# Optimization experiments

Hardware: AMD Instinct MI355X
Metric: run time of the kernel (lower is better)

The kernel has to match this reference:

```python
import jax, jax.numpy as jnp
import numpy as np

NPERSEG = 128  # filter_size


def setup_inputs() -> dict:
    key = jax.random.key(0)
    x = jax.random.normal(key, (32, 64, 16384), dtype=jnp.float32)
    return {"x": x}


def _welch_psd(x):
    # window=None -> rectangular, scaling = sum(ones^2) = NPERSEG, fs = 1.0
    step = NPERSEG // 2          # noverlap = nperseg // 2
    T = x.shape[-1]
    num_segments = (T - step) // step
    # frame the signal: [B, C, S, NPERSEG]
    idx = jnp.arange(num_segments)[:, None] * step + jnp.arange(NPERSEG)
    segs = x[..., idx]
    segs = segs - jnp.mean(segs, axis=-1, keepdims=True)
    seg_fft = jnp.fft.rfft(segs, axis=-1)
    psd = (jnp.abs(seg_fft) ** 2) / NPERSEG
    # nperseg even -> double all bins except DC and Nyquist
    factor = jnp.ones((psd.shape[-1],), dtype=psd.dtype).at[1:-1].set(2.0)
    psd = psd * factor
    return jnp.mean(psd, axis=-2)  # average over segments -> [B, C, F]


def reference(x):
    psd = _welch_psd(x)                       # [B, C, F], F = 65
    F_bins = psd.shape[-1]
    sqrt_psd = jnp.sqrt(psd)
    # weights = 1 / F (faithful to original: divides by psd.shape[-1])
    barycenter = jnp.sum(sqrt_psd / F_bins, axis=0) ** 2   # [C, F] (first_iter)
    D = jnp.sqrt(barycenter)[None] / sqrt_psd              # [B, C, F]
    H = jnp.fft.irfft(D, axis=-1)                          # [B, C, 2*(F-1)=128]
    H = jnp.fft.fftshift(H, axes=-1)
    H = jnp.flip(H, axis=-1)
    B, C, T = x.shape
    K = H.shape[-1]
    # per-sample depthwise conv1d, padding='same' (torch even-kernel: left=(K-1)//2, right=K-1-left)
    left = (K - 1) // 2
    out = jax.lax.conv_general_dilated(
        x.reshape(1, B * C, T),
        H.reshape(B * C, 1, K),
        window_strides=(1,),
        padding=[(left, K - 1 - left)],
        feature_group_count=B * C,
    )
    return out.reshape(B, C, T)
```

## Files before the change

kernel.cpp:

```cpp
#include <hip/hip_runtime.h>
#include <math.h>

#define NCH   2048
#define TLEN  16384
#define NSEG  255
#define NF    65

__device__ __forceinline__ int swzA(int i) {
    return (i & ~63) | ((i & 63) ^ ((i >> 6) & 31));
}
__host__ __device__ constexpr int br6(int i) {
    return ((i & 1) << 5) | ((i & 2) << 3) | ((i & 4) << 1) |
           ((i & 8) >> 1) | ((i & 16) >> 3) | ((i & 32) >> 5);
}

__attribute__((amdgpu_flat_work_group_size(256, 256), amdgpu_waves_per_eu(2, 2)))
__global__ void psd_kernel(const float* __restrict__ x, float* __restrict__ psd_g) {
    __shared__ float xl[TLEN];
    const int ch  = blockIdx.x;
    const int tid = threadIdx.x;
    const float4* __restrict__ x4 = reinterpret_cast<const float4*>(x) + (size_t)ch * (TLEN / 4);
#pragma unroll
    for (int it = 0; it < 16; ++it) {
        int i4 = it * 256 + tid;
        float4 v = x4[i4];
        int i = i4 << 2;
        xl[swzA(i + 0)] = v.x;
        xl[swzA(i + 1)] = v.y;
        xl[swzA(i + 2)] = v.z;
        xl[swzA(i + 3)] = v.w;
    }
    __syncthreads();

    const int   seg   = (tid < NSEG) ? tid : (NSEG - 1);
    const float valid = (tid < NSEG) ? 1.0f : 0.0f;
    const int   base  = seg * 64;

    float zr[64], zi[64];
#pragma unroll
    for (int i = 0; i < 64; ++i) {
        const int rb = br6(i);
        zr[i] = xl[swzA(base + 2 * rb)];
        zi[i] = xl[swzA(base + 2 * rb + 1)];
    }

    constexpr float STR[6] = {-1.0f, 0.0f, 0.70710678f, 0.92387953f, 0.98078528f, 0.99518473f};
    constexpr float STI[6] = {0.0f, -1.0f, -0.70710678f, -0.38268343f, -0.19509032f, -0.09801714f};
#pragma unroll
    for (int st = 0; st < 6; ++st) {
        const int m = 1 << st;
        float wr = 1.0f, wi = 0.0f;
#pragma unroll
        for (int j = 0; j < m; ++j) {
#pragma unroll
            for (int k = 0; k < 64; k += 2 * m) {
                const int a = k + j, b = a + m;
                float tr = wr * zr[b] - wi * zi[b];
                float ti = wr * zi[b] + wi * zr[b];
                zr[b] = zr[a] - tr; zi[b] = zi[a] - ti;
                zr[a] += tr;        zi[a] += ti;
            }
            float nwr = wr * STR[st] - wi * STI[st];
            wi = wr * STI[st] + wi * STR[st];
            wr = nwr;
        }
    }

    float vals[64];
    float p64;
    const float INV128 = 1.0f / 128.0f;
    {
        float v0 = zr[0] + zi[0];
        vals[0] = v0 * v0 * INV128 * valid;
        float v1 = zr[0] - zi[0];
        p64 = v1 * v1 * INV128 * valid;
        vals[32] = (zr[32] * zr[32] + zi[32] * zi[32]) * (2.0f * INV128) * valid;
    }
    float Wr = 0.9987954562f, Wi = -0.0490676743f;
#pragma unroll
    for (int k = 1; k < 32; ++k) {
        float ar = 0.5f * (zr[k] + zr[64 - k]);
        float ai = 0.5f * (zi[k] - zi[64 - k]);
        float br_ = 0.5f * (zi[k] + zi[64 - k]);
        float bi_ = 0.5f * (zr[64 - k] - zr[k]);
        float tr = Wr * br_ - Wi * bi_;
        float ti = Wr * bi_ + Wi * br_;
        float e1r = ar + tr, e1i = ai + ti;
        float e2r = ar - tr, e2i = ai - ti;
        vals[k]      = (e1r * e1r + e1i * e1i) * (2.0f * INV128) * valid;
        vals[64 - k] = (e2r * e2r + e2i * e2i) * (2.0f * INV128) * valid;
        float nWr = Wr * 0.9987954562f - Wi * (-0.0490676743f);
        Wi = Wr * (-0.0490676743f) + Wi * 0.9987954562f;
        Wr = nWr;
    }

    const int lane = tid & 63;
#define RSTAGE(m)                                                    \
    {                                                                \
        const bool hi = (lane & (m)) != 0;                           \
        _Pragma("unroll")                                            \
        for (int j = 0; j < (m); ++j) {                              \
            float a = vals[j], b = vals[j + (m)];                    \
            float t = __shfl_xor(hi ? a : b, (m));                   \
            vals[j] = (hi ? b : a) + t;                              \
        }                                                            \
    }
    RSTAGE(32) RSTAGE(16) RSTAGE(8) RSTAGE(4) RSTAGE(2) RSTAGE(1)
#undef RSTAGE
    p64 += __shfl_xor(p64, 32);
    p64 += __shfl_xor(p64, 16);
    p64 += __shfl_xor(p64, 8);
    p64 += __shfl_xor(p64, 4);
    p64 += __shfl_xor(p64, 2);
    p64 += __shfl_xor(p64, 1);

    float* pg = psd_g + ch * NF;
    atomicAdd(&pg[lane], vals[0]);
    if (lane == 0) atomicAdd(&pg[64], p64);
}

__launch_bounds__(256)
__global__ void sqrtp_kernel(const float* __restrict__ psd_g, float* __restrict__ sqrtP,
                             float* __restrict__ S) {
    int id = blockIdx.x * 256 + threadIdx.x;
    if (id >= 64 * NF) return;
    int c = id / NF, f = id - c * NF;
    float sum = 0.0f;
    for (int b = 0; b < 32; ++b) {
        int ch = (b << 6) + c;
        float sp = sqrtf(psd_g[ch * NF + f] * (1.0f / 255.0f));
        sqrtP[ch * NF + f] = sp;
        sum += sp;
    }
    S[id] = sum * (1.0f / 65.0f);
}

__launch_bounds__(128)
__global__ void filt_kernel(const float* __restrict__ sqrtP, const float* __restrict__ S,
                            float* __restrict__ h2g) {
    __shared__ float Dl[NF];
    const int ch = blockIdx.x;
    const int c  = ch & 63;
    const int n  = threadIdx.x;
    if (n < NF) {
        if (n == 0) {
            Dl[0] = 32.0f / 65.0f;
        } else {
            float sp = sqrtP[ch * NF + n];
            float sv = S[c * NF + n];
            Dl[n] = (sp > 0.0f) ? sv / sp : 0.0f;
        }
    }
    __syncthreads();
    float sum = Dl[0] + ((n & 1) ? -Dl[64] : Dl[64]);
#pragma unroll
    for (int f = 1; f < 64; ++f) {
        int m = (f * n) & 127;
        sum += 2.0f * Dl[f] * cosf((float)m * 0.04908738521f);
    }
    float h = sum * (1.0f / 128.0f);
    h2g[ch * 128 + ((n + 63) & 127)] = h;
}

#define CTILE 4096
#define CHALO 160
#define XTN   (CTILE + CHALO)

__device__ __forceinline__ int swz4(int j) { return j ^ ((j >> 3) & 7); }

__attribute__((amdgpu_flat_work_group_size(256, 256), amdgpu_waves_per_eu(4, 4)))
__global__ void conv_kernel(const float* __restrict__ x, const float* __restrict__ h2g,
                            float* __restrict__ out) {
    __shared__ __align__(16) float xt[XTN];
    __shared__ __align__(16) float H3[136];
    const int bid = blockIdx.x;
    const int ch  = bid >> 2;
    const int t0  = (bid & 3) * CTILE;
    const int tid = threadIdx.x;
    const float* __restrict__ xrow = x + (size_t)ch * TLEN;
    for (int i = tid; i < XTN; i += 256) {
        int src = t0 - 64 + i;
        float v = (src >= 0 && src < TLEN) ? xrow[src] : 0.0f;
        int j = i >> 2;
        xt[(swz4(j) << 2) | (i & 3)] = v;
    }
    if (tid < 136) {
        H3[tid] = (tid >= 1 && tid <= 128) ? h2g[ch * 128 + tid - 1] : 0.0f;
    }
    __syncthreads();

    float acc[16];
#pragma unroll
    for (int j = 0; j < 16; ++j) acc[j] = 0.0f;
    float xw[20];
    const float4* xt4 = reinterpret_cast<const float4*>(xt);
    const float4* H34 = reinterpret_cast<const float4*>(H3);
    const int jb = tid << 2;
#pragma unroll
    for (int c = 0; c < 5; ++c) {
        float4 v = xt4[swz4(jb + c)];
        xw[4 * c + 0] = v.x; xw[4 * c + 1] = v.y; xw[4 * c + 2] = v.z; xw[4 * c + 3] = v.w;
    }
#pragma unroll
    for (int cb = 0; cb < 33; ++cb) {
        const int kb = 4 * cb;
        float4 hv = H34[cb];
#pragma unroll
        for (int dk = 0; dk < 4; ++dk) {
            const float h = (dk == 0) ? hv.x : (dk == 1) ? hv.y : (dk == 2) ? hv.z : hv.w;
#pragma unroll
            for (int j = 0; j < 16; ++j) {
                acc[j] = fmaf(xw[(kb + dk + j) % 20], h, acc[j]);
            }
        }
        if (cb < 32) {
            float4 v = xt4[swz4(jb + cb + 5)];
            xw[(4 * cb + 0) % 20] = v.x;
            xw[(4 * cb + 1) % 20] = v.y;
            xw[(4 * cb + 2) % 20] = v.z;
            xw[(4 * cb + 3) % 20] = v.w;
        }
    }
    float4* o4 = reinterpret_cast<float4*>(out + (size_t)ch * TLEN + t0 + (tid << 4));
#pragma unroll
    for (int q = 0; q < 4; ++q) {
        o4[q] = make_float4(acc[4 * q + 0], acc[4 * q + 1], acc[4 * q + 2], acc[4 * q + 3]);
    }
}

extern "C" void kernel_launch(void* const* d_in, const int* in_sizes, int n_in,
                              void* d_out, int out_size, void* d_ws, size_t ws_size,
                              hipStream_t stream) {
    (void)in_sizes; (void)n_in; (void)out_size; (void)ws_size;
    const float* x = (const float*)d_in[0];
    float* out = (float*)d_out;
    char* ws = (char*)d_ws;
    float* psd_g = (float*)(ws);
    float* sqrtP = (float*)(ws + 532480);
    float* S     = (float*)(ws + 1064960);
    float* h2g   = (float*)(ws + 1081600);

    hipMemsetAsync(psd_g, 0, 532480, stream);
    psd_kernel <<<NCH,     256, 0, stream>>>(x, psd_g);
    sqrtp_kernel<<<17,     256, 0, stream>>>(psd_g, sqrtP, S);
    filt_kernel<<<NCH,     128, 0, stream>>>(sqrtP, S, h2g);
    conv_kernel<<<NCH * 4, 256, 0, stream>>>(x, h2g, out);
}
```

Baseline: 348.7 us.

## Run depthwise conv on MFMA with split-bf16 Toeplitz and drop PSD atomics

The FIR convolution is recast as a Toeplitz matrix product on bf16 MFMA instructions. Both the filter taps and the signal are split into high and low bf16 parts, and three MFMA products approximate fp32 accuracy. This replaces the scalar FMA loop. Separately, the PSD kernel now reduces across its four waves in shared memory and writes each channel directly, which removes the atomics and the memset. The split-bf16 scheme drops the lo*lo term, which adds a small precision risk.

```diff
diff --git a/kernel.cpp b/kernel.cpp
--- a/kernel.cpp
+++ b/kernel.cpp
@@ -5,6 +5,19 @@
 #define TLEN  16384
 #define NSEG  255
 #define NF    65
+
+typedef __attribute__((ext_vector_type(8))) short bf16x8;
+typedef __attribute__((ext_vector_type(4))) float f32x4;
+
+__device__ __forceinline__ unsigned short f2bf(float f) {
+    union { float f; unsigned u; } v; v.f = f;
+    unsigned r = v.u + 0x7FFF + ((v.u >> 16) & 1);
+    return (unsigned short)(r >> 16);
+}
+__device__ __forceinline__ float bf2f(unsigned short b) {
+    union { unsigned u; float f; } v; v.u = ((unsigned)b) << 16;
+    return v.f;
+}
 
 __device__ __forceinline__ int swzA(int i) {
     return (i & ~63) | ((i & 63) ^ ((i >> 6) & 31));
@@ -19,6 +32,8 @@
     __shared__ float xl[TLEN];
     const int ch  = blockIdx.x;
     const int tid = threadIdx.x;
+    const int lane = tid & 63;
+    const int w    = tid >> 6;
     const float4* __restrict__ x4 = reinterpret_cast<const float4*>(x) + (size_t)ch * (TLEN / 4);
 #pragma unroll
     for (int it = 0; it < 16; ++it) {
@@ -94,10 +109,10 @@
         Wr = nWr;
     }
 
-    const int lane = tid & 63;
+    const int l = lane;
 #define RSTAGE(m)                                                    \
     {                                                                \
-        const bool hi = (lane & (m)) != 0;                           \
+        const bool hi = (l & (m)) != 0;                              \
         _Pragma("unroll")                                            \
         for (int j = 0; j < (m); ++j) {                              \
             float a = vals[j], b = vals[j + (m)];                    \
@@ -114,9 +129,17 @@
     p64 += __shfl_xor(p64, 2);
     p64 += __shfl_xor(p64, 1);
 
-    float* pg = psd_g + ch * NF;
-    atomicAdd(&pg[lane], vals[0]);
-    if (lane == 0) atomicAdd(&pg[64], p64);
+    __syncthreads();
+    float* red = xl;
+    red[w * 80 + lane] = vals[0];
+    if (lane == 0) red[320 + w] = p64;
+    __syncthreads();
+    if (tid < NF) {
+        float s;
+        if (tid < 64) s = red[tid] + red[80 + tid] + red[160 + tid] + red[240 + tid];
+        else          s = red[320] + red[321] + red[322] + red[323];
+        psd_g[ch * NF + tid] = s;
+    }
 }
 
 __launch_bounds__(256)
@@ -162,69 +185,88 @@
     h2g[ch * 128 + ((n + 63) & 127)] = h;
 }
 
-#define CTILE 4096
-#define CHALO 160
-#define XTN   (CTILE + CHALO)
-
-__device__ __forceinline__ int swz4(int j) { return j ^ ((j >> 3) & 7); }
+#define BS    4096
+#define KPAD  160
+#define XU    (BS + KPAD)
+#define PHYS(u) ((u) + (((u) >> 4) << 2))
 
 __attribute__((amdgpu_flat_work_group_size(256, 256), amdgpu_waves_per_eu(4, 4)))
 __global__ void conv_kernel(const float* __restrict__ x, const float* __restrict__ h2g,
                             float* __restrict__ out) {
-    __shared__ __align__(16) float xt[XTN];
-    __shared__ __align__(16) float H3[136];
-    const int bid = blockIdx.x;
-    const int ch  = bid >> 2;
-    const int t0  = (bid & 3) * CTILE;
-    const int tid = threadIdx.x;
+    __shared__ __align__(16) unsigned short Xh[PHYS(XU)];
+    __shared__ __align__(16) unsigned short Xl[PHYS(XU)];
+    const int bid  = blockIdx.x;
+    const int ch   = bid >> 2;
+    const int t0   = (bid & 3) * BS;
+    const int tid  = threadIdx.x;
+    const int lane = tid & 63;
+    const int w    = tid >> 6;
     const float* __restrict__ xrow = x + (size_t)ch * TLEN;
-    for (int i = tid; i < XTN; i += 256) {
-        int src = t0 - 64 + i;
-        float v = (src >= 0 && src < TLEN) ? xrow[src] : 0.0f;
-        int j = i >> 2;
-        xt[(swz4(j) << 2) | (i & 3)] = v;
-    }
-    if (tid < 136) {
-        H3[tid] = (tid >= 1 && tid <= 128) ? h2g[ch * 128 + tid - 1] : 0.0f;
-    }
-    __syncthreads();
-
-    float acc[16];
-#pragma unroll
-    for (int j = 0; j < 16; ++j) acc[j] = 0.0f;
-    float xw[20];
-    const float4* xt4 = reinterpret_cast<const float4*>(xt);
-    const float4* H34 = reinterpret_cast<const float4*>(H3);
-    const int jb = tid << 2;
-#pragma unroll
-    for (int c = 0; c < 5; ++c) {
-        float4 v = xt4[swz4(jb + c)];
-        xw[4 * c + 0] = v.x; xw[4 * c + 1] = v.y; xw[4 * c + 2] = v.z; xw[4 * c + 3] = v.w;
-    }
-#pragma unroll
-    for (int cb = 0; cb < 33; ++cb) {
-        const int kb = 4 * cb;
-        float4 hv = H34[cb];
-#pragma unroll
-        for (int dk = 0; dk < 4; ++dk) {
-            const float h = (dk == 0) ? hv.x : (dk == 1) ? hv.y : (dk == 2) ? hv.z : hv.w;
-#pragma unroll
-            for (int j = 0; j < 16; ++j) {
-                acc[j] = fmaf(xw[(kb + dk + j) % 20], h, acc[j]);
+
+    bf16x8 Ah[5], Al[5];
+    {
+        const float* __restrict__ hrow = h2g + ch * 128;
+        const int r  = lane & 15;
+        const int kg = (lane >> 4) << 2;
+#pragma unroll
+        for (int c = 0; c < 5; ++c) {
+#pragma unroll
+            for (int e = 0; e < 8; ++e) {
+                int idx = 32 * c + kg + (e & 3) + ((e >> 2) << 4) - r - 1;
+                float hv = (idx >= 0 && idx < 128) ? hrow[idx] : 0.0f;
+                unsigned short hh = f2bf(hv);
+                Ah[c][e] = (short)hh;
+                Al[c][e] = (short)f2bf(hv - bf2f(hh));
             }
         }
-        if (cb < 32) {
-            float4 v = xt4[swz4(jb + cb + 5)];
-            xw[(4 * cb + 0) % 20] = v.x;
-            xw[(4 * cb + 1) % 20] = v.y;
-            xw[(4 * cb + 2) % 20] = v.z;
-            xw[(4 * cb + 3) % 20] = v.w;
-        }
-    }
-    float4* o4 = reinterpret_cast<float4*>(out + (size_t)ch * TLEN + t0 + (tid << 4));
+    }
+
+    for (int i4 = tid; i4 < XU / 4; i4 += 256) {
+        int u0  = i4 << 2;
+        int src = t0 - 64 + u0;
+        float4 v;
+        if (src >= 0 && src + 3 < TLEN) {
+            v = *reinterpret_cast<const float4*>(xrow + src);
+        } else {
+            v.x = (src + 0 >= 0 && src + 0 < TLEN) ? xrow[src + 0] : 0.0f;
+            v.y = (src + 1 >= 0 && src + 1 < TLEN) ? xrow[src + 1] : 0.0f;
+            v.z = (src + 2 >= 0 && src + 2 < TLEN) ? xrow[src + 2] : 0.0f;
+            v.w = (src + 3 >= 0 && src + 3 < TLEN) ? xrow[src + 3] : 0.0f;
+        }
+        ushort4 hi, lo;
+        hi.x = f2bf(v.x); lo.x = f2bf(v.x - bf2f(hi.x));
+        hi.y = f2bf(v.y); lo.y = f2bf(v.y - bf2f(hi.y));
+        hi.z = f2bf(v.z); lo.z = f2bf(v.z - bf2f(hi.z));
+        hi.w = f2bf(v.w); lo.w = f2bf(v.w - bf2f(hi.w));
+        int p = PHYS(u0);
+        *reinterpret_cast<ushort4*>(Xh + p) = hi;
+        *reinterpret_cast<ushort4*>(Xl + p) = lo;
+    }
+    __syncthreads();
+
+    const int ub0 = 16 * (lane & 15) + ((lane >> 4) << 2);
 #pragma unroll
     for (int q = 0; q < 4; ++q) {
-        o4[q] = make_float4(acc[4 * q + 0], acc[4 * q + 1], acc[4 * q + 2], acc[4 * q + 3]);
+        const int tb = 256 * (w + (q << 2));
+        f32x4 acc = {0.0f, 0.0f, 0.0f, 0.0f};
+#pragma unroll
+        for (int c = 0; c < 5; ++c) {
+            int p0 = PHYS(ub0 + tb + 32 * c);
+            ushort4 h0 = *reinterpret_cast<const ushort4*>(Xh + p0);
+            ushort4 h1 = *reinterpret_cast<const ushort4*>(Xh + p0 + 20);
+            ushort4 l0 = *reinterpret_cast<const ushort4*>(Xl + p0);
+            ushort4 l1 = *reinterpret_cast<const ushort4*>(Xl + p0 + 20);
+            bf16x8 bh = {(short)h0.x, (short)h0.y, (short)h0.z, (short)h0.w,
+                         (short)h1.x, (short)h1.y, (short)h1.z, (short)h1.w};
+            bf16x8 bl = {(short)l0.x, (short)l0.y, (short)l0.z, (short)l0.w,
+                         (short)l1.x, (short)l1.y, (short)l1.z, (short)l1.w};
+            acc = __builtin_amdgcn_mfma_f32_16x16x32_bf16(Ah[c], bh, acc, 0, 0, 0);
+            acc = __builtin_amdgcn_mfma_f32_16x16x32_bf16(Ah[c], bl, acc, 0, 0, 0);
+            acc = __builtin_amdgcn_mfma_f32_16x16x32_bf16(Al[c], bh, acc, 0, 0, 0);
+        }
+        float* orow = out + (size_t)ch * TLEN + t0 + tb
+                    + 16 * (lane & 15) + ((lane >> 4) << 2);
+        *reinterpret_cast<float4*>(orow) = make_float4(acc[0], acc[1], acc[2], acc[3]);
     }
 }
 
@@ -240,7 +282,6 @@
     float* S     = (float*)(ws + 1064960);
     float* h2g   = (float*)(ws + 1081600);
 
-    hipMemsetAsync(psd_g, 0, 532480, stream);
     psd_kernel <<<NCH,     256, 0, stream>>>(x, psd_g);
     sqrtp_kernel<<<17,     256, 0, stream>>>(psd_g, sqrtP, S);
     filt_kernel<<<NCH,     128, 0, stream>>>(sqrtP, S, h2g);
```

Result: faster. 292.6 us (-16.1%).
